# Kernel tuning notes

Hardware: AMD Instinct MI355X
Metric: run time of the kernel (lower is better)

The kernel has to match this reference:

```python
import jax, jax.numpy as jnp
import numpy as np

B, C_IN, N = 32, 64, 128
OUT_FEATS = (64, 64, 128)
ATT_DIM = 64
EPS = 1e-5  # torch BatchNorm default


def _bn(x, g, b, m, v):
    # eval-mode BatchNorm over channel axis 1 (running stats m, v)
    shape = (1, -1) + (1,) * (x.ndim - 2)
    inv = g / jnp.sqrt(v + EPS)
    return (x - m.reshape(shape)) * inv.reshape(shape) + b.reshape(shape)


def setup_inputs() -> dict:
    key = jax.random.key(0)
    ks = iter(jax.random.split(key, 48))

    def w(shape, scale=0.05):
        return jax.random.normal(next(ks), shape, jnp.float32) * scale

    inp = {"features": jax.random.normal(next(ks), (B, C_IN, N), jnp.float32)}
    in_dims = (2 * C_IN, OUT_FEATS[0], OUT_FEATS[1])
    for li in range(3):
        o, ci = OUT_FEATS[li], in_dims[li]
        inp[f"w{li}"] = w((o, ci))                  # Conv2d 1x1, no bias (BN)
        inp[f"g{li}"] = 1.0 + w((o,))               # BN gamma
        inp[f"b{li}"] = w((o,))                     # BN beta
        inp[f"m{li}"] = w((o,))                     # BN running mean
        inp[f"v{li}"] = 1.0 + 0.1 * jax.random.uniform(next(ks), (o,), jnp.float32)
    inp["wa0"] = w((ATT_DIM, OUT_FEATS[-1]))        # attention conv (no bias)
    inp["ga"] = 1.0 + w((ATT_DIM,))
    inp["ba"] = w((ATT_DIM,))
    inp["ma"] = w((ATT_DIM,))
    inp["va"] = 1.0 + 0.1 * jax.random.uniform(next(ks), (ATT_DIM,), jnp.float32)
    inp["wa1"] = w((1, ATT_DIM))                    # final attention conv (bias)
    inp["ba1"] = w((1,))
    inp["wsc"] = w((OUT_FEATS[-1], C_IN))           # shortcut Conv1d (no bias)
    inp["gsc"] = 1.0 + w((OUT_FEATS[-1],))
    inp["bsc"] = w((OUT_FEATS[-1],))
    inp["msc"] = w((OUT_FEATS[-1],))
    inp["vsc"] = 1.0 + 0.1 * jax.random.uniform(next(ks), (OUT_FEATS[-1],), jnp.float32)
    return inp


def reference(features, w0, g0, b0, m0, v0, w1, g1, b1, m1, v1,
              w2, g2, b2, m2, v2, wa0, ga, ba, ma, va, wa1, ba1,
              wsc, gsc, bsc, msc, vsc):
    n = features.shape[-1]
    # neighbor index table: row i lists all j != i, shape (N, N-1)
    base = jnp.broadcast_to(jnp.arange(n)[None, :], (n, n))
    idx = jnp.where(base >= jnp.arange(n)[:, None], base + 1, base)[:, :-1]
    x_i = features[:, :, :, None]                   # (B,C,N,1)
    x_j = features[:, :, idx]                       # (B,C,N,N-1) gather
    x = jnp.concatenate([jnp.broadcast_to(x_i, x_j.shape), x_j - x_i], axis=1)  # (B,2C,N,N-1)
    for w_, g_, b_, m_, v_ in ((w0, g0, b0, m0, v0), (w1, g1, b1, m1, v1), (w2, g2, b2, m2, v2)):
        x = jnp.einsum('oc,bcnk->bonk', w_, x)      # 1x1 conv
        x = jax.nn.relu(_bn(x, g_, b_, m_, v_))
    # attention pooling over neighbor axis k
    a = jax.nn.relu(_bn(jnp.einsum('oc,bcnk->bonk', wa0, x), ga, ba, ma, va))
    logits = jnp.einsum('oc,bcnk->bonk', wa1, a) + ba1.reshape(1, 1, 1, 1)
    attw = jax.nn.softmax(logits[:, 0], axis=-1)    # (B,N,N-1)
    fts = jnp.einsum('bcnk,bnk->bcn', x, attw)      # (B,C_out,N)
    # shortcut branch (in_feat != out_feats[-1])
    sc = _bn(jnp.einsum('oc,bcn->bon', wsc, features), gsc, bsc, msc, vsc)
    return jax.nn.relu(sc + fts)
```

## Files before the change

kernel.cpp:

```cpp
#include <hip/hip_runtime.h>

typedef unsigned short u16;
typedef short short8 __attribute__((ext_vector_type(8)));
typedef float floatx4 __attribute__((ext_vector_type(4)));

#define MFMA16(a, b, c) __builtin_amdgcn_mfma_f32_16x16x32_bf16((a), (b), (c), 0, 0, 0)

#define W1F_OFF   0u
#define B1F_OFF   8192u
#define W2F_OFF   8448u
#define B2F_OFF   24832u
#define WA0F_OFF  25344u
#define BAF_OFF   41728u
#define WA1F_OFF  41984u
#define BA1F_OFF  42240u
#define P_OFF     42496u
#define Q_OFF     1091072u
#define SC_OFF    2139648u
#define WS_TOTAL  4236800u

__device__ __align__(256) char g_ws[WS_TOTAL];

#define LD0 72
#define LD2 136

__device__ __forceinline__ float bits2f(unsigned u) {
  union { unsigned i; float f; } v; v.i = u; return v.f;
}
__device__ __forceinline__ u16 f2bf(float f) {
  union { float f; unsigned i; } v; v.f = f;
  return (u16)((v.i + 0x8000u) >> 16);
}

__global__ __launch_bounds__(256) void k_pre(
    const float* __restrict__ feat, const float* __restrict__ w0,
    const float* __restrict__ g0, const float* __restrict__ b0, const float* __restrict__ m0, const float* __restrict__ v0,
    const float* __restrict__ w1, const float* __restrict__ g1, const float* __restrict__ b1, const float* __restrict__ m1, const float* __restrict__ v1,
    const float* __restrict__ w2, const float* __restrict__ g2, const float* __restrict__ b2, const float* __restrict__ m2, const float* __restrict__ v2,
    const float* __restrict__ wa0, const float* __restrict__ ga, const float* __restrict__ ba, const float* __restrict__ ma, const float* __restrict__ va,
    const float* __restrict__ wa1, const float* __restrict__ ba1,
    const float* __restrict__ wsc, const float* __restrict__ gsc, const float* __restrict__ bsc, const float* __restrict__ msc, const float* __restrict__ vsc)
{
  __shared__ float smem[9600];
  const int t = threadIdx.x;
  char* ws = g_ws;
  const int blk = blockIdx.x;

  if (blk == 512) {
    float* fs1 = smem; float* fs2 = smem + 64; float* fsa = smem + 192;
    if (t < 64) {
      float s;
      s = g1[t] * rsqrtf(v1[t] + 1e-5f); fs1[t] = s; ((float*)(ws + B1F_OFF))[t] = b1[t] - m1[t] * s;
      s = ga[t] * rsqrtf(va[t] + 1e-5f); fsa[t] = s; ((float*)(ws + BAF_OFF))[t] = ba[t] - ma[t] * s;
      ((float*)(ws + WA1F_OFF))[t] = wa1[t];
    }
    if (t < 128) { float s = g2[t] * rsqrtf(v2[t] + 1e-5f); fs2[t] = s; ((float*)(ws + B2F_OFF))[t] = b2[t] - m2[t] * s; }
    if (t == 0) ((float*)(ws + BA1F_OFF))[0] = ba1[0];
    __syncthreads();
    u16* W1f = (u16*)(ws + W1F_OFF);
    u16* W2f = (u16*)(ws + W2F_OFF);
    u16* Wa0f = (u16*)(ws + WA0F_OFF);
    for (int i = t; i < 4096; i += 256) W1f[i]  = f2bf(fs1[i >> 6] * w1[i]);
    for (int i = t; i < 8192; i += 256) W2f[i]  = f2bf(fs2[i >> 6] * w2[i]);
    for (int i = t; i < 8192; i += 256) Wa0f[i] = f2bf(fsa[i >> 7] * wa0[i]);
    return;
  }

  const int sub = blk & 255;
  const int b = sub >> 3, n0 = (sub & 7) << 4;
  float* Xs  = smem;
  float* Wsm = smem + 1280;

  {
    const int c = t >> 2, j = (t & 3) << 2;
    *(float4*)(Xs + c * 20 + j) = *(const float4*)(feat + b * 8192 + c * 128 + n0 + j);
  }

  if (blk < 256) {
    #pragma unroll
    for (int r = 0; r < 8; r++) {
      const int i = (r * 256 + t) * 4;
      float4 v = *(const float4*)(w0 + i);
      const int o = i >> 7, c = i & 127;
      float* d = Wsm + o * 129 + c;
      d[0] = v.x; d[1] = v.y; d[2] = v.z; d[3] = v.w;
    }
    __syncthreads();
    const int o = t & 63, nb = (t >> 6) << 2;
    const float s  = g0[o] * rsqrtf(v0[o] + 1e-5f);
    const float tt = b0[o] - m0[o] * s;
    const float* wr = Wsm + o * 129;
    float dA0=0.f,dA1=0.f,dA2=0.f,dA3=0.f,dB0=0.f,dB1=0.f,dB2=0.f,dB3=0.f;
    #pragma unroll
    for (int c = 0; c < 64; c++) {
      const float a = wr[c], e = wr[64 + c];
      const float4 x = *(const float4*)(Xs + c * 20 + nb);
      dA0 += a * x.x; dA1 += a * x.y; dA2 += a * x.z; dA3 += a * x.w;
      dB0 += e * x.x; dB1 += e * x.y; dB2 += e * x.z; dB3 += e * x.w;
    }
    float* Pp = (float*)(ws + P_OFF) + (b * 128 + n0 + nb) * 64 + o;
    float* Qp = (float*)(ws + Q_OFF) + (b * 128 + n0 + nb) * 64 + o;
    Pp[0]   = s * dB0; Pp[64]  = s * dB1; Pp[128] = s * dB2; Pp[192] = s * dB3;
    Qp[0]   = s * (dA0 - dB0) + tt; Qp[64]  = s * (dA1 - dB1) + tt;
    Qp[128] = s * (dA2 - dB2) + tt; Qp[192] = s * (dA3 - dB3) + tt;
  } else {
    #pragma unroll
    for (int r = 0; r < 8; r++) {
      const int i = (r * 256 + t) * 4;
      float4 v = *(const float4*)(wsc + i);
      const int o = i >> 6, c = i & 63;
      float* d = Wsm + o * 65 + c;
      d[0] = v.x; d[1] = v.y; d[2] = v.z; d[3] = v.w;
    }
    __syncthreads();
    const int o = t & 127, h = (t >> 7) << 3;
    const float s  = gsc[o] * rsqrtf(vsc[o] + 1e-5f);
    const float tt = bsc[o] - msc[o] * s;
    const float* wr = Wsm + o * 65;
    float d0=0.f,d1=0.f,d2=0.f,d3=0.f,d4=0.f,d5=0.f,d6=0.f,d7=0.f;
    #pragma unroll
    for (int c = 0; c < 64; c++) {
      const float a = wr[c];
      const float4 x0 = *(const float4*)(Xs + c * 20 + h);
      const float4 x1 = *(const float4*)(Xs + c * 20 + h + 4);
      d0 += a * x0.x; d1 += a * x0.y; d2 += a * x0.z; d3 += a * x0.w;
      d4 += a * x1.x; d5 += a * x1.y; d6 += a * x1.z; d7 += a * x1.w;
    }
    float* SCp = (float*)(ws + SC_OFF) + (b * 128 + n0 + h) * 128 + o;
    SCp[0]   = s * d0 + tt; SCp[128] = s * d1 + tt; SCp[256] = s * d2 + tt; SCp[384] = s * d3 + tt;
    SCp[512] = s * d4 + tt; SCp[640] = s * d5 + tt; SCp[768] = s * d6 + tt; SCp[896] = s * d7 + tt;
  }
}

__global__ __launch_bounds__(256, 4) void k_main(float* __restrict__ out)
{
  __shared__ alignas(16) u16 buf[18432];
  __shared__ float parts[4][128];
  __shared__ float attws[128];

  const int blk = blockIdx.x, b = blk >> 7, n = blk & 127, t = threadIdx.x;
  const char* ws = g_ws;
  const float* Pb  = (const float*)(ws + P_OFF);
  const float* Qb  = (const float*)(ws + Q_OFF);
  const float* SCb = (const float*)(ws + SC_OFF);
  const u16*   W1f = (const u16*)(ws + W1F_OFF);
  const float* b1f = (const float*)(ws + B1F_OFF);
  const u16*   W2f = (const u16*)(ws + W2F_OFF);
  const float* b2f = (const float*)(ws + B2F_OFF);
  const u16*   Wa0f= (const u16*)(ws + WA0F_OFF);
  const float* baf = (const float*)(ws + BAF_OFF);
  const float* wa1f= (const float*)(ws + WA1F_OFF);
  const float  ba1v= *(const float*)(ws + BA1F_OFF);

  u16* H0 = buf;
  u16* H1 = buf + 9216;
  u16* H2 = buf;

  const int lane = t & 63, wid = t >> 6, quad = lane >> 4, l16 = lane & 15;
  const int koff = quad * 8;

  const short8 a1w0 = *(const short8*)(W1f + (wid * 16 + l16) * 64 + koff);
  const short8 a1w1 = *(const short8*)(W1f + (wid * 16 + l16) * 64 + 32 + koff);
  const short8 a2w00 = *(const short8*)(W2f + (wid * 32 + l16) * 64 + koff);
  const short8 a2w01 = *(const short8*)(W2f + (wid * 32 + l16) * 64 + 32 + koff);
  const short8 a2w10 = *(const short8*)(W2f + (wid * 32 + 16 + l16) * 64 + koff);
  const short8 a2w11 = *(const short8*)(W2f + (wid * 32 + 16 + l16) * 64 + 32 + koff);

  {
    const int k = t >> 1, half = t & 1;
    const int j = (k < 127) ? ((k < n) ? k : (k + 1)) : n;
    const float4* pr = (const float4*)(Pb + ((b << 7) + j) * 64 + half * 32);
    const float4* qr = (const float4*)(Qb + blk * 64 + half * 32);
    u16* dst = H0 + k * LD0 + half * 32;
    #pragma unroll
    for (int i = 0; i < 8; i++) {
      float4 p = pr[i], q = qr[i];
      ushort4 sv;
      sv.x = f2bf(fmaxf(q.x + p.x, 0.f));
      sv.y = f2bf(fmaxf(q.y + p.y, 0.f));
      sv.z = f2bf(fmaxf(q.z + p.z, 0.f));
      sv.w = f2bf(fmaxf(q.w + p.w, 0.f));
      *(ushort4*)(dst + i * 4) = sv;
    }
  }
  __syncthreads();

  {
    floatx4 acc[8];
    #pragma unroll
    for (int et = 0; et < 8; et++) acc[et] = (floatx4)(0.f);
    #pragma unroll
    for (int et = 0; et < 8; et++) {
      const u16* br = H0 + (et * 16 + l16) * LD0 + koff;
      short8 bf0 = *(const short8*)(br);
      short8 bf1 = *(const short8*)(br + 32);
      acc[et] = MFMA16(a1w0, bf0, acc[et]);
      acc[et] = MFMA16(a1w1, bf1, acc[et]);
    }
    const int r0 = wid * 16 + quad * 4;
    const float4 bb = *(const float4*)(b1f + r0);
    #pragma unroll
    for (int et = 0; et < 8; et++) {
      ushort4 sv;
      sv.x = f2bf(fmaxf(acc[et][0] + bb.x, 0.f));
      sv.y = f2bf(fmaxf(acc[et][1] + bb.y, 0.f));
      sv.z = f2bf(fmaxf(acc[et][2] + bb.z, 0.f));
      sv.w = f2bf(fmaxf(acc[et][3] + bb.w, 0.f));
      *(ushort4*)(H1 + (et * 16 + l16) * LD0 + r0) = sv;
    }
  }
  __syncthreads();

  {
    floatx4 acc[2][8];
    #pragma unroll
    for (int m = 0; m < 2; m++)
      #pragma unroll
      for (int et = 0; et < 8; et++) acc[m][et] = (floatx4)(0.f);
    #pragma unroll
    for (int et = 0; et < 8; et++) {
      const u16* br = H1 + (et * 16 + l16) * LD0 + koff;
      short8 bf0 = *(const short8*)(br);
      short8 bf1 = *(const short8*)(br + 32);
      acc[0][et] = MFMA16(a2w00, bf0, acc[0][et]);
      acc[0][et] = MFMA16(a2w01, bf1, acc[0][et]);
      acc[1][et] = MFMA16(a2w10, bf0, acc[1][et]);
      acc[1][et] = MFMA16(a2w11, bf1, acc[1][et]);
    }
    __syncthreads();
    #pragma unroll
    for (int m = 0; m < 2; m++) {
      const int r0 = wid * 32 + m * 16 + quad * 4;
      const float4 bb = *(const float4*)(b2f + r0);
      #pragma unroll
      for (int et = 0; et < 8; et++) {
        ushort4 sv;
        sv.x = f2bf(fmaxf(acc[m][et][0] + bb.x, 0.f));
        sv.y = f2bf(fmaxf(acc[m][et][1] + bb.y, 0.f));
        sv.z = f2bf(fmaxf(acc[m][et][2] + bb.z, 0.f));
        sv.w = f2bf(fmaxf(acc[m][et][3] + bb.w, 0.f));
        *(ushort4*)(H2 + (et * 16 + l16) * LD2 + r0) = sv;
      }
    }
  }
  __syncthreads();

  float scv = 0.f;
  if (t < 128) scv = SCb[blk * 128 + t];
  float* outp = out + ((b << 7) + (t & 127)) * 128 + n;

  {
    short8 a3[4];
    #pragma unroll
    for (int ks = 0; ks < 4; ks++)
      a3[ks] = *(const short8*)(Wa0f + (wid * 16 + l16) * 128 + ks * 32 + koff);
    floatx4 acc[8];
    #pragma unroll
    for (int et = 0; et < 8; et++) acc[et] = (floatx4)(0.f);
    #pragma unroll
    for (int et = 0; et < 8; et++) {
      const u16* br = H2 + (et * 16 + l16) * LD2 + koff;
      #pragma unroll
      for (int ks = 0; ks < 4; ks++) {
        short8 bf = *(const short8*)(br + ks * 32);
        acc[et] = MFMA16(a3[ks], bf, acc[et]);
      }
    }
    const int r0 = wid * 16 + quad * 4;
    const float4 wv = *(const float4*)(wa1f + r0);
    const float4 bb = *(const float4*)(baf + r0);
    #pragma unroll
    for (int et = 0; et < 8; et++) {
      float p = wv.x * fmaxf(acc[et][0] + bb.x, 0.f) + wv.y * fmaxf(acc[et][1] + bb.y, 0.f)
              + wv.z * fmaxf(acc[et][2] + bb.z, 0.f) + wv.w * fmaxf(acc[et][3] + bb.w, 0.f);
      p += __shfl_xor(p, 16); p += __shfl_xor(p, 32);
      if (quad == 0) parts[wid][et * 16 + l16] = p;
    }
  }
  __syncthreads();

  if (wid == 0) {
    float a0 = parts[0][lane] + parts[1][lane] + parts[2][lane] + parts[3][lane] + ba1v;
    float a1 = (lane == 63) ? -1e30f
             : (parts[0][lane + 64] + parts[1][lane + 64] + parts[2][lane + 64] + parts[3][lane + 64] + ba1v);
    float mx = fmaxf(a0, a1);
    #pragma unroll
    for (int off = 32; off >= 1; off >>= 1) mx = fmaxf(mx, __shfl_xor(mx, off));
    float e0 = expf(a0 - mx), e1 = expf(a1 - mx);
    float sm = e0 + e1;
    #pragma unroll
    for (int off = 32; off >= 1; off >>= 1) sm += __shfl_xor(sm, off);
    float inv = 1.f / sm;
    attws[lane] = e0 * inv;
    attws[lane + 64] = e1 * inv;
  }
  __syncthreads();

  {
    const int chg = t & 15, eg = t >> 4;
    float fa[8];
    #pragma unroll
    for (int k = 0; k < 8; k++) fa[k] = 0.f;
    #pragma unroll
    for (int i = 0; i < 8; i++) {
      const int e = eg * 8 + i;
      const float w = attws[e];
      uint4 v = *(const uint4*)(H2 + e * LD2 + chg * 8);
      unsigned u;
      u = v.x; fa[0] += w * bits2f(u << 16); fa[1] += w * bits2f(u & 0xffff0000u);
      u = v.y; fa[2] += w * bits2f(u << 16); fa[3] += w * bits2f(u & 0xffff0000u);
      u = v.z; fa[4] += w * bits2f(u << 16); fa[5] += w * bits2f(u & 0xffff0000u);
      u = v.w; fa[6] += w * bits2f(u << 16); fa[7] += w * bits2f(u & 0xffff0000u);
    }
    #pragma unroll
    for (int k = 0; k < 8; k++) { fa[k] += __shfl_xor(fa[k], 16); fa[k] += __shfl_xor(fa[k], 32); }
    if (lane < 16) {
      #pragma unroll
      for (int k = 0; k < 8; k++) parts[wid][chg * 8 + k] = fa[k];
    }
  }
  __syncthreads();

  if (t < 128) {
    float fts = parts[0][t] + parts[1][t] + parts[2][t] + parts[3][t];
    *outp = fmaxf(scv + fts, 0.f);
  }
}

extern "C" void kernel_launch(void* const* d_in, const int* in_sizes, int n_in,
                              void* d_out, int out_size, void* d_ws, size_t ws_size,
                              hipStream_t stream)
{
  (void)d_ws; (void)ws_size; (void)in_sizes; (void)n_in; (void)out_size;
  const float* feat = (const float*)d_in[0];
  const float *w0 = (const float*)d_in[1],  *g0 = (const float*)d_in[2],  *b0 = (const float*)d_in[3],  *m0 = (const float*)d_in[4],  *v0 = (const float*)d_in[5];
  const float *w1 = (const float*)d_in[6],  *g1 = (const float*)d_in[7],  *b1 = (const float*)d_in[8],  *m1 = (const float*)d_in[9],  *v1 = (const float*)d_in[10];
  const float *w2 = (const float*)d_in[11], *g2 = (const float*)d_in[12], *b2 = (const float*)d_in[13], *m2 = (const float*)d_in[14], *v2 = (const float*)d_in[15];
  const float *wa0= (const float*)d_in[16], *ga = (const float*)d_in[17], *ba = (const float*)d_in[18], *ma = (const float*)d_in[19], *va = (const float*)d_in[20];
  const float *wa1= (const float*)d_in[21], *ba1= (const float*)d_in[22];
  const float *wsc= (const float*)d_in[23], *gsc= (const float*)d_in[24], *bsc= (const float*)d_in[25], *msc= (const float*)d_in[26], *vsc= (const float*)d_in[27];

  k_pre<<<dim3(513), dim3(256), 0, stream>>>(
      feat, w0, g0, b0, m0, v0, w1, g1, b1, m1, v1, w2, g2, b2, m2, v2,
      wa0, ga, ba, ma, va, wa1, ba1, wsc, gsc, bsc, msc, vsc);
  k_main<<<dim3(4096), dim3(256), 0, stream>>>((float*)d_out);
}
```

Measured before the change: 172.8 us.

## Fuse precompute kernel into main kernel with per-block MFMA neighbor projection

Removes the separate precompute kernel and its global workspace. Each block now folds the BN scales into its bf16 weight fragments directly from the fp32 inputs. It also computes the first layer's neighbor term for all 128 points with MFMA on a bf16 copy of the features in LDS, and computes the centre term and shortcut branch locally. This avoids a second launch and the round trip of the P/Q/SC intermediates through global memory. In exchange every block redoes the per-batch projection and the weight folding, which adds redundant compute and L2 traffic for weight reads.

```diff
diff --git a/kernel.cpp b/kernel.cpp
--- a/kernel.cpp
+++ b/kernel.cpp
@@ -6,21 +6,6 @@
 
 #define MFMA16(a, b, c) __builtin_amdgcn_mfma_f32_16x16x32_bf16((a), (b), (c), 0, 0, 0)
 
-#define W1F_OFF   0u
-#define B1F_OFF   8192u
-#define W2F_OFF   8448u
-#define B2F_OFF   24832u
-#define WA0F_OFF  25344u
-#define BAF_OFF   41728u
-#define WA1F_OFF  41984u
-#define BA1F_OFF  42240u
-#define P_OFF     42496u
-#define Q_OFF     1091072u
-#define SC_OFF    2139648u
-#define WS_TOTAL  4236800u
-
-__device__ __align__(256) char g_ws[WS_TOTAL];
-
 #define LD0 72
 #define LD2 136
 
@@ -31,158 +16,168 @@
   union { float f; unsigned i; } v; v.f = f;
   return (u16)((v.i + 0x8000u) >> 16);
 }
-
-__global__ __launch_bounds__(256) void k_pre(
+__device__ __forceinline__ short8 foldpack(const float* __restrict__ p, float s) {
+  float4 u = *(const float4*)p, v = *(const float4*)(p + 4);
+  short8 r;
+  r[0] = (short)f2bf(s * u.x); r[1] = (short)f2bf(s * u.y);
+  r[2] = (short)f2bf(s * u.z); r[3] = (short)f2bf(s * u.w);
+  r[4] = (short)f2bf(s * v.x); r[5] = (short)f2bf(s * v.y);
+  r[6] = (short)f2bf(s * v.z); r[7] = (short)f2bf(s * v.w);
+  return r;
+}
+
+__global__ __launch_bounds__(256, 4) void k_fused(
     const float* __restrict__ feat, const float* __restrict__ w0,
     const float* __restrict__ g0, const float* __restrict__ b0, const float* __restrict__ m0, const float* __restrict__ v0,
     const float* __restrict__ w1, const float* __restrict__ g1, const float* __restrict__ b1, const float* __restrict__ m1, const float* __restrict__ v1,
     const float* __restrict__ w2, const float* __restrict__ g2, const float* __restrict__ b2, const float* __restrict__ m2, const float* __restrict__ v2,
     const float* __restrict__ wa0, const float* __restrict__ ga, const float* __restrict__ ba, const float* __restrict__ ma, const float* __restrict__ va,
     const float* __restrict__ wa1, const float* __restrict__ ba1,
-    const float* __restrict__ wsc, const float* __restrict__ gsc, const float* __restrict__ bsc, const float* __restrict__ msc, const float* __restrict__ vsc)
-{
-  __shared__ float smem[9600];
-  const int t = threadIdx.x;
-  char* ws = g_ws;
-  const int blk = blockIdx.x;
-
-  if (blk == 512) {
-    float* fs1 = smem; float* fs2 = smem + 64; float* fsa = smem + 192;
-    if (t < 64) {
-      float s;
-      s = g1[t] * rsqrtf(v1[t] + 1e-5f); fs1[t] = s; ((float*)(ws + B1F_OFF))[t] = b1[t] - m1[t] * s;
-      s = ga[t] * rsqrtf(va[t] + 1e-5f); fsa[t] = s; ((float*)(ws + BAF_OFF))[t] = ba[t] - ma[t] * s;
-      ((float*)(ws + WA1F_OFF))[t] = wa1[t];
-    }
-    if (t < 128) { float s = g2[t] * rsqrtf(v2[t] + 1e-5f); fs2[t] = s; ((float*)(ws + B2F_OFF))[t] = b2[t] - m2[t] * s; }
-    if (t == 0) ((float*)(ws + BA1F_OFF))[0] = ba1[0];
-    __syncthreads();
-    u16* W1f = (u16*)(ws + W1F_OFF);
-    u16* W2f = (u16*)(ws + W2F_OFF);
-    u16* Wa0f = (u16*)(ws + WA0F_OFF);
-    for (int i = t; i < 4096; i += 256) W1f[i]  = f2bf(fs1[i >> 6] * w1[i]);
-    for (int i = t; i < 8192; i += 256) W2f[i]  = f2bf(fs2[i >> 6] * w2[i]);
-    for (int i = t; i < 8192; i += 256) Wa0f[i] = f2bf(fsa[i >> 7] * wa0[i]);
-    return;
-  }
-
-  const int sub = blk & 255;
-  const int b = sub >> 3, n0 = (sub & 7) << 4;
-  float* Xs  = smem;
-  float* Wsm = smem + 1280;
-
-  {
-    const int c = t >> 2, j = (t & 3) << 2;
-    *(float4*)(Xs + c * 20 + j) = *(const float4*)(feat + b * 8192 + c * 128 + n0 + j);
-  }
-
-  if (blk < 256) {
-    #pragma unroll
-    for (int r = 0; r < 8; r++) {
-      const int i = (r * 256 + t) * 4;
-      float4 v = *(const float4*)(w0 + i);
-      const int o = i >> 7, c = i & 127;
-      float* d = Wsm + o * 129 + c;
-      d[0] = v.x; d[1] = v.y; d[2] = v.z; d[3] = v.w;
-    }
-    __syncthreads();
-    const int o = t & 63, nb = (t >> 6) << 2;
-    const float s  = g0[o] * rsqrtf(v0[o] + 1e-5f);
-    const float tt = b0[o] - m0[o] * s;
-    const float* wr = Wsm + o * 129;
-    float dA0=0.f,dA1=0.f,dA2=0.f,dA3=0.f,dB0=0.f,dB1=0.f,dB2=0.f,dB3=0.f;
-    #pragma unroll
-    for (int c = 0; c < 64; c++) {
-      const float a = wr[c], e = wr[64 + c];
-      const float4 x = *(const float4*)(Xs + c * 20 + nb);
-      dA0 += a * x.x; dA1 += a * x.y; dA2 += a * x.z; dA3 += a * x.w;
-      dB0 += e * x.x; dB1 += e * x.y; dB2 += e * x.z; dB3 += e * x.w;
-    }
-    float* Pp = (float*)(ws + P_OFF) + (b * 128 + n0 + nb) * 64 + o;
-    float* Qp = (float*)(ws + Q_OFF) + (b * 128 + n0 + nb) * 64 + o;
-    Pp[0]   = s * dB0; Pp[64]  = s * dB1; Pp[128] = s * dB2; Pp[192] = s * dB3;
-    Qp[0]   = s * (dA0 - dB0) + tt; Qp[64]  = s * (dA1 - dB1) + tt;
-    Qp[128] = s * (dA2 - dB2) + tt; Qp[192] = s * (dA3 - dB3) + tt;
-  } else {
-    #pragma unroll
-    for (int r = 0; r < 8; r++) {
-      const int i = (r * 256 + t) * 4;
-      float4 v = *(const float4*)(wsc + i);
-      const int o = i >> 6, c = i & 63;
-      float* d = Wsm + o * 65 + c;
-      d[0] = v.x; d[1] = v.y; d[2] = v.z; d[3] = v.w;
-    }
-    __syncthreads();
-    const int o = t & 127, h = (t >> 7) << 3;
-    const float s  = gsc[o] * rsqrtf(vsc[o] + 1e-5f);
-    const float tt = bsc[o] - msc[o] * s;
-    const float* wr = Wsm + o * 65;
-    float d0=0.f,d1=0.f,d2=0.f,d3=0.f,d4=0.f,d5=0.f,d6=0.f,d7=0.f;
-    #pragma unroll
-    for (int c = 0; c < 64; c++) {
-      const float a = wr[c];
-      const float4 x0 = *(const float4*)(Xs + c * 20 + h);
-      const float4 x1 = *(const float4*)(Xs + c * 20 + h + 4);
-      d0 += a * x0.x; d1 += a * x0.y; d2 += a * x0.z; d3 += a * x0.w;
-      d4 += a * x1.x; d5 += a * x1.y; d6 += a * x1.z; d7 += a * x1.w;
-    }
-    float* SCp = (float*)(ws + SC_OFF) + (b * 128 + n0 + h) * 128 + o;
-    SCp[0]   = s * d0 + tt; SCp[128] = s * d1 + tt; SCp[256] = s * d2 + tt; SCp[384] = s * d3 + tt;
-    SCp[512] = s * d4 + tt; SCp[640] = s * d5 + tt; SCp[768] = s * d6 + tt; SCp[896] = s * d7 + tt;
-  }
-}
-
-__global__ __launch_bounds__(256, 4) void k_main(float* __restrict__ out)
+    const float* __restrict__ wsc, const float* __restrict__ gsc, const float* __restrict__ bsc, const float* __restrict__ msc, const float* __restrict__ vsc,
+    float* __restrict__ out)
 {
   __shared__ alignas(16) u16 buf[18432];
   __shared__ float parts[4][128];
   __shared__ float attws[128];
+  __shared__ alignas(16) float xns[64];
 
   const int blk = blockIdx.x, b = blk >> 7, n = blk & 127, t = threadIdx.x;
-  const char* ws = g_ws;
-  const float* Pb  = (const float*)(ws + P_OFF);
-  const float* Qb  = (const float*)(ws + Q_OFF);
-  const float* SCb = (const float*)(ws + SC_OFF);
-  const u16*   W1f = (const u16*)(ws + W1F_OFF);
-  const float* b1f = (const float*)(ws + B1F_OFF);
-  const u16*   W2f = (const u16*)(ws + W2F_OFF);
-  const float* b2f = (const float*)(ws + B2F_OFF);
-  const u16*   Wa0f= (const u16*)(ws + WA0F_OFF);
-  const float* baf = (const float*)(ws + BAF_OFF);
-  const float* wa1f= (const float*)(ws + WA1F_OFF);
-  const float  ba1v= *(const float*)(ws + BA1F_OFF);
-
+  const int lane = t & 63, wid = t >> 6, quad = lane >> 4, l16 = lane & 15;
+  const int koff = quad * 8;
+  const float* featb = feat + b * 8192;
+
+  u16* Xw = buf + 9216;
   u16* H0 = buf;
   u16* H1 = buf + 9216;
   u16* H2 = buf;
 
-  const int lane = t & 63, wid = t >> 6, quad = lane >> 4, l16 = lane & 15;
-  const int koff = quad * 8;
-
-  const short8 a1w0 = *(const short8*)(W1f + (wid * 16 + l16) * 64 + koff);
-  const short8 a1w1 = *(const short8*)(W1f + (wid * 16 + l16) * 64 + 32 + koff);
-  const short8 a2w00 = *(const short8*)(W2f + (wid * 32 + l16) * 64 + koff);
-  const short8 a2w01 = *(const short8*)(W2f + (wid * 32 + l16) * 64 + 32 + koff);
-  const short8 a2w10 = *(const short8*)(W2f + (wid * 32 + 16 + l16) * 64 + koff);
-  const short8 a2w11 = *(const short8*)(W2f + (wid * 32 + 16 + l16) * 64 + 32 + koff);
-
-  {
-    const int k = t >> 1, half = t & 1;
-    const int j = (k < 127) ? ((k < n) ? k : (k + 1)) : n;
-    const float4* pr = (const float4*)(Pb + ((b << 7) + j) * 64 + half * 32);
-    const float4* qr = (const float4*)(Qb + blk * 64 + half * 32);
-    u16* dst = H0 + k * LD0 + half * 32;
-    #pragma unroll
-    for (int i = 0; i < 8; i++) {
-      float4 p = pr[i], q = qr[i];
+  const int ch = wid * 16 + l16;
+  const float s1r = g1[ch] * rsqrtf(v1[ch] + 1e-5f);
+  const short8 a1w0 = foldpack(w1 + ch * 64 + koff, s1r);
+  const short8 a1w1 = foldpack(w1 + ch * 64 + 32 + koff, s1r);
+  const int ch2a = wid * 32 + l16, ch2b = ch2a + 16;
+  const float s2a = g2[ch2a] * rsqrtf(v2[ch2a] + 1e-5f);
+  const float s2b = g2[ch2b] * rsqrtf(v2[ch2b] + 1e-5f);
+  const short8 a2w00 = foldpack(w2 + ch2a * 64 + koff, s2a);
+  const short8 a2w01 = foldpack(w2 + ch2a * 64 + 32 + koff, s2a);
+  const short8 a2w10 = foldpack(w2 + ch2b * 64 + koff, s2b);
+  const short8 a2w11 = foldpack(w2 + ch2b * 64 + 32 + koff, s2b);
+  const float s0r = g0[ch] * rsqrtf(v0[ch] + 1e-5f);
+  const short8 a0f0 = foldpack(w0 + ch * 128 + 64 + koff, s0r);
+  const short8 a0f1 = foldpack(w0 + ch * 128 + 64 + 32 + koff, s0r);
+
+  const int r0 = wid * 16 + quad * 4;
+  float4 bb1, bb2a, bb2b, bbA, wv;
+  {
+    float4 gv = *(const float4*)(g1 + r0), bv = *(const float4*)(b1 + r0);
+    float4 mv = *(const float4*)(m1 + r0), vv = *(const float4*)(v1 + r0);
+    bb1.x = bv.x - mv.x * gv.x * rsqrtf(vv.x + 1e-5f);
+    bb1.y = bv.y - mv.y * gv.y * rsqrtf(vv.y + 1e-5f);
+    bb1.z = bv.z - mv.z * gv.z * rsqrtf(vv.z + 1e-5f);
+    bb1.w = bv.w - mv.w * gv.w * rsqrtf(vv.w + 1e-5f);
+  }
+  {
+    const int r2 = wid * 32 + quad * 4;
+    float4 gv = *(const float4*)(g2 + r2), bv = *(const float4*)(b2 + r2);
+    float4 mv = *(const float4*)(m2 + r2), vv = *(const float4*)(v2 + r2);
+    bb2a.x = bv.x - mv.x * gv.x * rsqrtf(vv.x + 1e-5f);
+    bb2a.y = bv.y - mv.y * gv.y * rsqrtf(vv.y + 1e-5f);
+    bb2a.z = bv.z - mv.z * gv.z * rsqrtf(vv.z + 1e-5f);
+    bb2a.w = bv.w - mv.w * gv.w * rsqrtf(vv.w + 1e-5f);
+    gv = *(const float4*)(g2 + r2 + 16); bv = *(const float4*)(b2 + r2 + 16);
+    mv = *(const float4*)(m2 + r2 + 16); vv = *(const float4*)(v2 + r2 + 16);
+    bb2b.x = bv.x - mv.x * gv.x * rsqrtf(vv.x + 1e-5f);
+    bb2b.y = bv.y - mv.y * gv.y * rsqrtf(vv.y + 1e-5f);
+    bb2b.z = bv.z - mv.z * gv.z * rsqrtf(vv.z + 1e-5f);
+    bb2b.w = bv.w - mv.w * gv.w * rsqrtf(vv.w + 1e-5f);
+  }
+  {
+    float4 gv = *(const float4*)(ga + r0), bv = *(const float4*)(ba + r0);
+    float4 mv = *(const float4*)(ma + r0), vv = *(const float4*)(va + r0);
+    bbA.x = bv.x - mv.x * gv.x * rsqrtf(vv.x + 1e-5f);
+    bbA.y = bv.y - mv.y * gv.y * rsqrtf(vv.y + 1e-5f);
+    bbA.z = bv.z - mv.z * gv.z * rsqrtf(vv.z + 1e-5f);
+    bbA.w = bv.w - mv.w * gv.w * rsqrtf(vv.w + 1e-5f);
+    wv = *(const float4*)(wa1 + r0);
+  }
+  const float ba1v = ba1[0];
+
+  {
+    const int c0 = (t & 15) * 4, j0 = (t >> 4) * 8;
+    #pragma unroll
+    for (int jj = 0; jj < 8; jj += 4) {
+      float4 f0 = *(const float4*)(featb + (c0 + 0) * 128 + j0 + jj);
+      float4 f1 = *(const float4*)(featb + (c0 + 1) * 128 + j0 + jj);
+      float4 f2 = *(const float4*)(featb + (c0 + 2) * 128 + j0 + jj);
+      float4 f3 = *(const float4*)(featb + (c0 + 3) * 128 + j0 + jj);
+      ushort4 s0v = { f2bf(f0.x), f2bf(f1.x), f2bf(f2.x), f2bf(f3.x) };
+      ushort4 s1v = { f2bf(f0.y), f2bf(f1.y), f2bf(f2.y), f2bf(f3.y) };
+      ushort4 s2v = { f2bf(f0.z), f2bf(f1.z), f2bf(f2.z), f2bf(f3.z) };
+      ushort4 s3v = { f2bf(f0.w), f2bf(f1.w), f2bf(f2.w), f2bf(f3.w) };
+      *(ushort4*)(Xw + (j0 + jj + 0) * LD0 + c0) = s0v;
+      *(ushort4*)(Xw + (j0 + jj + 1) * LD0 + c0) = s1v;
+      *(ushort4*)(Xw + (j0 + jj + 2) * LD0 + c0) = s2v;
+      *(ushort4*)(Xw + (j0 + jj + 3) * LD0 + c0) = s3v;
+    }
+    if (t < 64) xns[t] = featb[t * 128 + n];
+  }
+  __syncthreads();
+
+  {
+    floatx4 pacc[8];
+    #pragma unroll
+    for (int jt = 0; jt < 8; jt++) pacc[jt] = (floatx4)(0.f);
+    #pragma unroll
+    for (int jt = 0; jt < 8; jt++) {
+      const u16* br = Xw + (jt * 16 + l16) * LD0 + koff;
+      short8 bf0 = *(const short8*)(br);
+      short8 bf1 = *(const short8*)(br + 32);
+      pacc[jt] = MFMA16(a0f0, bf0, pacc[jt]);
+      pacc[jt] = MFMA16(a0f1, bf1, pacc[jt]);
+    }
+    float qa = 0.f;
+    const float4* wr = (const float4*)(w0 + ch * 128);
+    #pragma unroll
+    for (int k4 = 0; k4 < 16; k4++) {
+      float4 wa = wr[k4], wbv = wr[16 + k4];
+      float4 x = *(const float4*)(xns + k4 * 4);
+      qa += (wa.x - wbv.x) * x.x + (wa.y - wbv.y) * x.y
+          + (wa.z - wbv.z) * x.z + (wa.w - wbv.w) * x.w;
+    }
+    const float qv = s0r * qa + (b0[ch] - m0[ch] * s0r);
+    float4 qf;
+    qf.x = __shfl(qv, quad * 20 + 0);
+    qf.y = __shfl(qv, quad * 20 + 1);
+    qf.z = __shfl(qv, quad * 20 + 2);
+    qf.w = __shfl(qv, quad * 20 + 3);
+    const int ch0 = wid * 16 + quad * 4;
+    #pragma unroll
+    for (int jt = 0; jt < 8; jt++) {
+      const int j = jt * 16 + l16;
+      const int k = (j < n) ? j : ((j > n) ? (j - 1) : 127);
       ushort4 sv;
-      sv.x = f2bf(fmaxf(q.x + p.x, 0.f));
-      sv.y = f2bf(fmaxf(q.y + p.y, 0.f));
-      sv.z = f2bf(fmaxf(q.z + p.z, 0.f));
-      sv.w = f2bf(fmaxf(q.w + p.w, 0.f));
-      *(ushort4*)(dst + i * 4) = sv;
-    }
-  }
+      sv.x = f2bf(fmaxf(qf.x + pacc[jt][0], 0.f));
+      sv.y = f2bf(fmaxf(qf.y + pacc[jt][1], 0.f));
+      sv.z = f2bf(fmaxf(qf.z + pacc[jt][2], 0.f));
+      sv.w = f2bf(fmaxf(qf.w + pacc[jt][3], 0.f));
+      *(ushort4*)(H0 + k * LD0 + ch0) = sv;
+    }
+  }
+  float scv = 0.f;
+  if (t < 128) {
+    const float ssc = gsc[t] * rsqrtf(vsc[t] + 1e-5f);
+    const float tsc = bsc[t] - msc[t] * ssc;
+    const float4* wr = (const float4*)(wsc + t * 64);
+    float d = 0.f;
+    #pragma unroll
+    for (int k4 = 0; k4 < 16; k4++) {
+      float4 a = wr[k4];
+      float4 x = *(const float4*)(xns + k4 * 4);
+      d += a.x * x.x + a.y * x.y + a.z * x.z + a.w * x.w;
+    }
+    scv = ssc * d + tsc;
+  }
+  float* outp = out + ((b << 7) + (t & 127)) * 128 + n;
   __syncthreads();
 
   {
@@ -197,16 +192,15 @@
       acc[et] = MFMA16(a1w0, bf0, acc[et]);
       acc[et] = MFMA16(a1w1, bf1, acc[et]);
     }
-    const int r0 = wid * 16 + quad * 4;
-    const float4 bb = *(const float4*)(b1f + r0);
+    const int rr = wid * 16 + quad * 4;
     #pragma unroll
     for (int et = 0; et < 8; et++) {
       ushort4 sv;
-      sv.x = f2bf(fmaxf(acc[et][0] + bb.x, 0.f));
-      sv.y = f2bf(fmaxf(acc[et][1] + bb.y, 0.f));
-      sv.z = f2bf(fmaxf(acc[et][2] + bb.z, 0.f));
-      sv.w = f2bf(fmaxf(acc[et][3] + bb.w, 0.f));
-      *(ushort4*)(H1 + (et * 16 + l16) * LD0 + r0) = sv;
+      sv.x = f2bf(fmaxf(acc[et][0] + bb1.x, 0.f));
+      sv.y = f2bf(fmaxf(acc[et][1] + bb1.y, 0.f));
+      sv.z = f2bf(fmaxf(acc[et][2] + bb1.z, 0.f));
+      sv.w = f2bf(fmaxf(acc[et][3] + bb1.w, 0.f));
+      *(ushort4*)(H1 + (et * 16 + l16) * LD0 + rr) = sv;
     }
   }
   __syncthreads();
@@ -230,8 +224,8 @@
     __syncthreads();
     #pragma unroll
     for (int m = 0; m < 2; m++) {
-      const int r0 = wid * 32 + m * 16 + quad * 4;
-      const float4 bb = *(const float4*)(b2f + r0);
+      const int rr = wid * 32 + m * 16 + quad * 4;
+      const float4 bb = m ? bb2b : bb2a;
       #pragma unroll
       for (int et = 0; et < 8; et++) {
         ushort4 sv;
@@ -239,21 +233,18 @@
         sv.y = f2bf(fmaxf(acc[m][et][1] + bb.y, 0.f));
         sv.z = f2bf(fmaxf(acc[m][et][2] + bb.z, 0.f));
         sv.w = f2bf(fmaxf(acc[m][et][3] + bb.w, 0.f));
-        *(ushort4*)(H2 + (et * 16 + l16) * LD2 + r0) = sv;
+        *(ushort4*)(H2 + (et * 16 + l16) * LD2 + rr) = sv;
       }
     }
   }
   __syncthreads();
 
-  float scv = 0.f;
-  if (t < 128) scv = SCb[blk * 128 + t];
-  float* outp = out + ((b << 7) + (t & 127)) * 128 + n;
-
-  {
+  {
+    const float sar = ga[ch] * rsqrtf(va[ch] + 1e-5f);
     short8 a3[4];
     #pragma unroll
     for (int ks = 0; ks < 4; ks++)
-      a3[ks] = *(const short8*)(Wa0f + (wid * 16 + l16) * 128 + ks * 32 + koff);
+      a3[ks] = foldpack(wa0 + ch * 128 + ks * 32 + koff, sar);
     floatx4 acc[8];
     #pragma unroll
     for (int et = 0; et < 8; et++) acc[et] = (floatx4)(0.f);
@@ -266,13 +257,10 @@
         acc[et] = MFMA16(a3[ks], bf, acc[et]);
       }
     }
-    const int r0 = wid * 16 + quad * 4;
-    const float4 wv = *(const float4*)(wa1f + r0);
-    const float4 bb = *(const float4*)(baf + r0);
-    #pragma unroll
-    for (int et = 0; et < 8; et++) {
-      float p = wv.x * fmaxf(acc[et][0] + bb.x, 0.f) + wv.y * fmaxf(acc[et][1] + bb.y, 0.f)
-              + wv.z * fmaxf(acc[et][2] + bb.z, 0.f) + wv.w * fmaxf(acc[et][3] + bb.w, 0.f);
+    #pragma unroll
+    for (int et = 0; et < 8; et++) {
+      float p = wv.x * fmaxf(acc[et][0] + bbA.x, 0.f) + wv.y * fmaxf(acc[et][1] + bbA.y, 0.f)
+              + wv.z * fmaxf(acc[et][2] + bbA.z, 0.f) + wv.w * fmaxf(acc[et][3] + bbA.w, 0.f);
       p += __shfl_xor(p, 16); p += __shfl_xor(p, 32);
       if (quad == 0) parts[wid][et * 16 + l16] = p;
     }
@@ -340,8 +328,7 @@
   const float *wa1= (const float*)d_in[21], *ba1= (const float*)d_in[22];
   const float *wsc= (const float*)d_in[23], *gsc= (const float*)d_in[24], *bsc= (const float*)d_in[25], *msc= (const float*)d_in[26], *vsc= (const float*)d_in[27];
 
-  k_pre<<<dim3(513), dim3(256), 0, stream>>>(
+  k_fused<<<dim3(4096), dim3(256), 0, stream>>>(
       feat, w0, g0, b0, m0, v0, w1, g1, b1, m1, v1, w2, g2, b2, m2, v2,
-      wa0, ga, ba, ma, va, wa1, ba1, wsc, gsc, bsc, msc, vsc);
-  k_main<<<dim3(4096), dim3(256), 0, stream>>>((float*)d_out);
-}
+      wa0, ga, ba, ma, va, wa1, ba1, wsc, gsc, bsc, msc, vsc, (float*)d_out);
+}
```

After: 323.2 us. +87.0%, slower.
